# Kernel optimization log

Hardware: AMD Instinct MI355X
Metric: run time of the kernel (lower is better)

Reference implementation:

```python
import jax, jax.numpy as jnp
import numpy as np


def _split_feature(x, ns):
    # channel-last split: [b,h,w,c] -> [b*ns*ns, h/ns, w/ns, c]
    b, h, w, c = x.shape
    hn, wn = h // ns, w // ns
    return x.reshape(b, ns, hn, ns, wn, c).transpose(0, 1, 3, 2, 4, 5).reshape(b * ns * ns, hn, wn, c)


def _merge_splits(x, ns):
    # inverse of _split_feature: [b*ns*ns, h, w, c] -> [b, ns*h, ns*w, c]
    b, h, w, c = x.shape
    nb = b // (ns * ns)
    return x.reshape(nb, ns, ns, h, w, c).transpose(0, 1, 3, 2, 4, 5).reshape(nb, ns * h, ns * w, c)


def _gen_shift_window_attn_mask(h, w, ns):
    # numpy replica of _unimatch_generate_shift_window_attn_mask
    wsh, wsw = h // ns, w // ns
    ssh, ssw = wsh // 2, wsw // 2
    img = np.zeros((1, h, w, 1), dtype=np.float32)
    cnt = 0
    for hs in (slice(0, -wsh), slice(-wsh, -ssh), slice(-ssh, None)):
        for ws in (slice(0, -wsw), slice(-wsw, -ssw), slice(-ssw, None)):
            img[:, hs, ws, :] = cnt
            cnt += 1
    win = img.reshape(1, ns, wsh, ns, wsw, 1).transpose(0, 1, 3, 2, 4, 5).reshape(ns * ns, wsh * wsw)
    am = win[:, None, :] - win[:, :, None]
    return np.where(am != 0, np.float32(-100.0), np.float32(0.0)).astype(np.float32)


def setup_inputs() -> dict:
    key = jax.random.key(0)
    B, H, W, C, NS = 8, 96, 128, 128, 4
    kq, kk, kv = jax.random.split(key, 3)
    q = jax.random.normal(kq, (B, H * W, C), jnp.float32)
    k = jax.random.normal(kk, (B, H * W, C), jnp.float32)
    v = jax.random.normal(kv, (B, H * W, C), jnp.float32)
    attn_mask = jnp.asarray(_gen_shift_window_attn_mask(H, W, NS))  # [NS*NS, n, n]
    return {"q": q, "k": k, "v": v, "attn_mask": attn_mask,
            "num_splits": NS, "with_shift": 1, "h": H, "w": W}


def reference(q, k, v, attn_mask, num_splits, with_shift, h, w):
    b, _, c = q.shape
    ns = num_splits
    wsh, wsw = h // ns, w // ns
    n = wsh * wsw
    bn = b * ns * ns
    q = q.reshape(b, h, w, c)
    k = k.reshape(b, h, w, c)
    v = v.reshape(b, h, w, c)
    if with_shift:
        sh, sw = wsh // 2, wsw // 2
        q = jnp.roll(q, (-sh, -sw), axis=(1, 2))
        k = jnp.roll(k, (-sh, -sw), axis=(1, 2))
        v = jnp.roll(v, (-sh, -sw), axis=(1, 2))
    qf = _split_feature(q, ns).reshape(bn, n, c)
    kf = _split_feature(k, ns).reshape(bn, n, c)
    vf = _split_feature(v, ns).reshape(bn, n, c)
    scale = jnp.asarray(c, qf.dtype) ** 0.5
    scores = jnp.einsum('bnc,bmc->bnm', qf, kf) / scale  # [bn, n, n]
    if with_shift:
        scores = scores + jnp.tile(attn_mask, (b, 1, 1))
    attn = jax.nn.softmax(scores, axis=-1)
    out = jnp.einsum('bnm,bmc->bnc', attn, vf)
    out = _merge_splits(out.reshape(bn, wsh, wsw, c), ns)  # [b, h, w, c]
    if with_shift:
        out = jnp.roll(out, (sh, sw), axis=(1, 2))
    return out.reshape(b, h * w, c)
```

## Files before the change

kernel.cpp:

```cpp
#include <hip/hip_runtime.h>

#define H 96
#define W 128
#define C 128
#define WSH 24
#define WSW 32
#define NTOK 768
#define SH 12
#define SW 16
#define KT 32
#define NKT 24
#define PSTR 40
#define TILE_USH 8192
#define WS_NEED (128L * NKT * TILE_USH * 2)

typedef __attribute__((ext_vector_type(8))) short short8;
typedef __attribute__((ext_vector_type(4))) float floatx4;

__device__ inline unsigned short f2bf(float f) {
  union { float f; unsigned u; } un; un.f = f;
  unsigned r = un.u + 0x7FFF + ((un.u >> 16) & 1);
  return (unsigned short)(r >> 16);
}

__device__ inline int tok_off(int tok, int wh, int ww) {
  int r = tok >> 5;
  int cc = tok & 31;
  int y = wh * WSH + r + SH; if (y >= H) y -= H;
  int x = ww * WSW + cc + SW; if (x >= W) x -= W;
  return y * W + x;
}

__device__ inline void gll16(const void* g, void* lds) {
  __builtin_amdgcn_global_load_lds(
      (const __attribute__((address_space(1))) unsigned int*)g,
      (__attribute__((address_space(3))) unsigned int*)lds, 16, 0, 0);
}

__global__ __launch_bounds__(256) void prep_kernel(const float* __restrict__ k,
                                                   const float* __restrict__ v,
                                                   unsigned short* __restrict__ ws) {
  __shared__ unsigned short Vlds[KT][136];
  const int bid = blockIdx.x;
  const int xcd = bid & 7;
  const int jj = bid >> 3;
  const int w = xcd * 16 + (jj & 15);
  const int kt = jj >> 4;
  const int batch = w >> 4, win = w & 15;
  const int wh = win >> 2, ww = win & 3;
  int y = wh * WSH + kt + SH; if (y >= H) y -= H;

  const int t = threadIdx.x;
  const int key = t >> 3;
  const int j = t & 7;
  const int c0 = j * 16;
  int x = ww * WSW + key + SW; if (x >= W) x -= W;
  const long src = ((long)batch * H * W + (long)y * W + x) * C + c0;
  unsigned short* tile = ws + ((long)w * NKT + kt) * TILE_USH;

  {
    const float* kp = k + src;
    short8 s0, s1;
#pragma unroll
    for (int i = 0; i < 2; ++i) {
      floatx4 a = *(const floatx4*)(kp + i * 8);
      floatx4 b = *(const floatx4*)(kp + i * 8 + 4);
      s0[i*4+0] = (short)f2bf(a[0]); s0[i*4+1] = (short)f2bf(a[1]);
      s0[i*4+2] = (short)f2bf(a[2]); s0[i*4+3] = (short)f2bf(a[3]);
      s1[i*4+0] = (short)f2bf(b[0]); s1[i*4+1] = (short)f2bf(b[1]);
      s1[i*4+2] = (short)f2bf(b[2]); s1[i*4+3] = (short)f2bf(b[3]);
    }
    short8 o0, o1;
    o0[0]=s0[0]; o0[1]=s0[1]; o0[2]=s0[2]; o0[3]=s0[3]; o0[4]=s1[0]; o0[5]=s1[1]; o0[6]=s1[2]; o0[7]=s1[3];
    o1[0]=s0[4]; o1[1]=s0[5]; o1[2]=s0[6]; o1[3]=s0[7]; o1[4]=s1[4]; o1[5]=s1[5]; o1[6]=s1[6]; o1[7]=s1[7];
    const int kc = j >> 1;
    const int q2 = (j & 1) * 2;
    const int half = key >> 4, keyh = key & 15;
    unsigned short* kout = tile + kc * 1024 + half * 512 + keyh * 8;
    *(short8*)(kout + (q2    ) * 128) = o0;
    *(short8*)(kout + (q2 + 1) * 128) = o1;
  }
  {
    const float* vp = v + src;
#pragma unroll
    for (int i = 0; i < 4; ++i) {
      floatx4 a = *(const floatx4*)(vp + i * 4);
      Vlds[key][c0 + i*4 + 0] = f2bf(a[0]);
      Vlds[key][c0 + i*4 + 1] = f2bf(a[1]);
      Vlds[key][c0 + i*4 + 2] = f2bf(a[2]);
      Vlds[key][c0 + i*4 + 3] = f2bf(a[3]);
    }
  }
  __syncthreads();
  {
    const int cb = t >> 5;
    const int rem = t & 31;
    const int col = rem >> 1, qh = rem & 1;
    const int ch = cb * 16 + col;
#pragma unroll
    for (int qs = 0; qs < 2; ++qs) {
      const int quad = qh * 2 + qs;
      short8 o;
#pragma unroll
      for (int i = 0; i < 8; ++i)
        o[i] = (short)Vlds[(i & 1) * 16 + quad * 4 + (i >> 1)][ch];
      *(short8*)(tile + 4096 + cb * 512 + (quad * 16 + col) * 8) = o;
    }
  }
}

__global__ __launch_bounds__(256, 2) void attn_main(const float* __restrict__ q,
                                                    const unsigned short* __restrict__ ws,
                                                    float* __restrict__ out) {
  __shared__ unsigned short Kv[3][TILE_USH];
  __shared__ unsigned short Ps[4][3][16 * PSTR];

  const int bid = blockIdx.x;
  const int x8 = bid & 7;
  const int i = bid >> 3;
  const int w = x8 * 16 + (i & 15);
  const int qb = i >> 4;
  const int batch = w >> 4, win = w & 15;
  const int wh = win >> 2, ww = win & 3;

  const int tid = threadIdx.x;
  const int wv = tid >> 6, lane = tid & 63;
  const int col = lane & 15, quad = lane >> 4;
  const long bbase = (long)batch * (H * W * C);
  const int qbase = qb * 192 + wv * 48;
  const int loff = lane * 8;

  const char* wtile = (const char*)(ws + (long)w * (NKT * TILE_USH));

  auto stage = [&](int buf, int kt) {
    const char* g = wtile + ((long)kt << 14);
#pragma unroll
    for (int c = 0; c < 4; ++c) {
      const int chunk = wv * 4 + c;
      gll16(g + chunk * 1024 + lane * 16, &Kv[buf][chunk * 512]);
    }
  };

  stage(0, 0);
  stage(1, 1);

  short8 qfrag[3][4];
#pragma unroll
  for (int s = 0; s < 3; ++s) {
    const int qtok = qbase + s * 16 + col;
    const float* qp = q + bbase + (long)tok_off(qtok, wh, ww) * C + quad * 8;
#pragma unroll
    for (int kc = 0; kc < 4; ++kc) {
      floatx4 a = *(const floatx4*)(qp + kc * 32);
      floatx4 b = *(const floatx4*)(qp + kc * 32 + 4);
      short8 v8;
      v8[0]=(short)f2bf(a[0]); v8[1]=(short)f2bf(a[1]); v8[2]=(short)f2bf(a[2]); v8[3]=(short)f2bf(a[3]);
      v8[4]=(short)f2bf(b[0]); v8[5]=(short)f2bf(b[1]); v8[6]=(short)f2bf(b[2]); v8[7]=(short)f2bf(b[3]);
      qfrag[s][kc] = v8;
    }
  }

  int qreg[3];
#pragma unroll
  for (int s = 0; s < 3; ++s) {
    int t0 = qbase + s * 16;
    int rr_s = t0 >> 5;
    int qh = (wh == 3) ? ((rr_s >= SH) ? 2 : 1) : 0;
    int qw = (ww == 3) ? ((t0 & 16) ? 2 : 1) : 0;
    qreg[s] = qh * 3 + qw;
  }
  const int cw0 = (ww == 3) ? 1 : 0, cw1 = (ww == 3) ? 2 : 0;
  const float MNEG = -144.2695041f;
  const float SC2 = 0.12751739f;

  floatx4 oacc[3][8];
#pragma unroll
  for (int s = 0; s < 3; ++s)
#pragma unroll
    for (int cb = 0; cb < 8; ++cb) oacc[s][cb] = (floatx4){0.f, 0.f, 0.f, 0.f};
  float lsum[3][4];
#pragma unroll
  for (int s = 0; s < 3; ++s)
#pragma unroll
    for (int r = 0; r < 4; ++r) lsum[s][r] = 0.f;

  asm volatile("s_waitcnt vmcnt(4)" ::: "memory");
  __builtin_amdgcn_s_barrier();

  int cur = 0;
  for (int kt = 0; kt < NKT; ++kt) {
    if (kt + 2 < NKT) {
      int b2 = cur + 2; if (b2 >= 3) b2 -= 3;
      stage(b2, kt + 2);
    }

    short8 kf0[4], kf1[4];
#pragma unroll
    for (int kc = 0; kc < 4; ++kc) {
      kf0[kc] = *(const short8*)&Kv[cur][kc * 1024 + loff];
      kf1[kc] = *(const short8*)&Kv[cur][kc * 1024 + 512 + loff];
    }

    const int khb = (wh == 3) ? ((kt >= SH) ? 6 : 3) : 0;
    const int kr0 = khb + cw0, kr1 = khb + cw1;

    floatx4 A0[3], A1[3];
#pragma unroll
    for (int s = 0; s < 3; ++s) {
      A0[s] = (floatx4){0.f, 0.f, 0.f, 0.f};
      A1[s] = (floatx4){0.f, 0.f, 0.f, 0.f};
    }
    __builtin_amdgcn_s_setprio(1);
#pragma unroll
    for (int kc = 0; kc < 4; ++kc)
#pragma unroll
      for (int s = 0; s < 3; ++s) {
        A0[s] = __builtin_amdgcn_mfma_f32_16x16x32_bf16(qfrag[s][kc], kf0[kc], A0[s], 0, 0, 0);
        A1[s] = __builtin_amdgcn_mfma_f32_16x16x32_bf16(qfrag[s][kc], kf1[kc], A1[s], 0, 0, 0);
      }
    __builtin_amdgcn_s_setprio(0);

    short8 vf[8];
#pragma unroll
    for (int cb = 0; cb < 8; ++cb)
      vf[cb] = *(const short8*)&Kv[cur][4096 + cb * 512 + loff];

    unsigned pkw[3][4];
#pragma unroll
    for (int s = 0; s < 3; ++s) {
      const float m0 = (qreg[s] == kr0) ? 0.f : MNEG;
      const float m1 = (qreg[s] == kr1) ? 0.f : MNEG;
#pragma unroll
      for (int r = 0; r < 4; ++r) {
        float p0 = __builtin_amdgcn_exp2f(fmaf(A0[s][r], SC2, m0));
        float p1 = __builtin_amdgcn_exp2f(fmaf(A1[s][r], SC2, m1));
        lsum[s][r] += p0 + p1;
        pkw[s][r] = (unsigned)f2bf(p0) | ((unsigned)f2bf(p1) << 16);
      }
    }

#pragma unroll
    for (int s = 0; s < 3; ++s)
#pragma unroll
      for (int r = 0; r < 4; ++r)
        *(unsigned*)&Ps[wv][s][(quad * 4 + r) * PSTR + 2 * col] = pkw[s][r];

    short8 pf[3];
#pragma unroll
    for (int s = 0; s < 3; ++s)
      pf[s] = *(const short8*)&Ps[wv][s][col * PSTR + quad * 8];

    __builtin_amdgcn_s_setprio(1);
#pragma unroll
    for (int cb = 0; cb < 8; ++cb)
#pragma unroll
      for (int s = 0; s < 3; ++s)
        oacc[s][cb] = __builtin_amdgcn_mfma_f32_16x16x32_bf16(pf[s], vf[cb], oacc[s][cb], 0, 0, 0);
    __builtin_amdgcn_s_setprio(0);

    if (kt + 1 < NKT) {
      if (kt + 2 < NKT) asm volatile("s_waitcnt vmcnt(4)" ::: "memory");
      else              asm volatile("s_waitcnt vmcnt(0)" ::: "memory");
      __builtin_amdgcn_s_barrier();
    }
    cur += 1; if (cur == 3) cur = 0;
  }

#pragma unroll
  for (int s = 0; s < 3; ++s)
#pragma unroll
    for (int r = 0; r < 4; ++r) {
      float l = lsum[s][r];
      l += __shfl_xor(l, 1); l += __shfl_xor(l, 2);
      l += __shfl_xor(l, 4); l += __shfl_xor(l, 8);
      float inv = 1.0f / l;
      int tok = qbase + s * 16 + quad * 4 + r;
      float* op = out + bbase + (long)tok_off(tok, wh, ww) * C + col;
#pragma unroll
      for (int cb = 0; cb < 8; ++cb) op[cb * 16] = oacc[s][cb][r] * inv;
    }
}

#define KSTRF 136
#define VSTRF 40
#define PSTRF 40
__global__ __launch_bounds__(256, 2) void attn_fallback(
    const float* __restrict__ q, const float* __restrict__ k,
    const float* __restrict__ v, const float* __restrict__ mask,
    float* __restrict__ out) {
  __shared__ unsigned short Ks[KT * KSTRF];
  __shared__ unsigned short Vtl[C * VSTRF];
  __shared__ unsigned short Psf[4][16 * PSTRF];
  const int qtile = blockIdx.x;
  const int beta  = blockIdx.y;
  const int batch = beta >> 4;
  const int win   = beta & 15;
  const int wh = win >> 2, ww = win & 3;
  const int tid = threadIdx.x;
  const int wave = tid >> 6, lane = tid & 63;
  const int col = lane & 15, quad = lane >> 4;
  const long bbase = (long)batch * (H * W * C);
  const int qtok = qtile * 64 + wave * 16 + col;
  const float* qp = q + bbase + (long)tok_off(qtok, wh, ww) * C + quad * 8;
  short8 qfrag[4];
#pragma unroll
  for (int kc = 0; kc < 4; ++kc) {
    floatx4 a = *(const floatx4*)(qp + kc * 32);
    floatx4 b = *(const floatx4*)(qp + kc * 32 + 4);
    short8 s;
    s[0]=f2bf(a[0]); s[1]=f2bf(a[1]); s[2]=f2bf(a[2]); s[3]=f2bf(a[3]);
    s[4]=f2bf(b[0]); s[5]=f2bf(b[1]); s[6]=f2bf(b[2]); s[7]=f2bf(b[3]);
    qfrag[kc] = s;
  }
  floatx4 oacc[8];
#pragma unroll
  for (int i = 0; i < 8; ++i) oacc[i] = (floatx4){0.f,0.f,0.f,0.f};
  float mrow[4], lrow[4];
#pragma unroll
  for (int r = 0; r < 4; ++r) { mrow[r] = -1e30f; lrow[r] = 0.f; }
  const int skey = tid >> 3;
  const int sch  = (tid & 7) * 4;
  const float invscale = 0.088388347648318447f;
  const float* maskw = mask + (long)win * (NTOK * NTOK);
  const int qrow_m = qtile * 64 + wave * 16 + quad * 4;
  for (int kt = 0; kt < NKT; ++kt) {
    const int ktok0 = kt * KT;
    const long srow = bbase + (long)tok_off(ktok0 + skey, wh, ww) * C;
    const float* kp = k + srow;
    const float* vp = v + srow;
    __syncthreads();
#pragma unroll
    for (int j = 0; j < 4; ++j) {
      floatx4 f = *(const floatx4*)(kp + sch + j * 32);
      unsigned lo = (unsigned)f2bf(f[0]) | ((unsigned)f2bf(f[1]) << 16);
      unsigned hi = (unsigned)f2bf(f[2]) | ((unsigned)f2bf(f[3]) << 16);
      *(uint2*)&Ks[skey * KSTRF + sch + j * 32] = make_uint2(lo, hi);
    }
#pragma unroll
    for (int j = 0; j < 4; ++j) {
      floatx4 f = *(const floatx4*)(vp + sch + j * 32);
      int chb = sch + j * 32;
      Vtl[(chb + 0) * VSTRF + skey] = f2bf(f[0]);
      Vtl[(chb + 1) * VSTRF + skey] = f2bf(f[1]);
      Vtl[(chb + 2) * VSTRF + skey] = f2bf(f[2]);
      Vtl[(chb + 3) * VSTRF + skey] = f2bf(f[3]);
    }
    __syncthreads();
    floatx4 s0 = (floatx4){0.f,0.f,0.f,0.f};
    floatx4 s1 = (floatx4){0.f,0.f,0.f,0.f};
#pragma unroll
    for (int kc = 0; kc < 4; ++kc) {
      short8 k0 = *(const short8*)&Ks[col * KSTRF + kc * 32 + quad * 8];
      short8 k1 = *(const short8*)&Ks[(col + 16) * KSTRF + kc * 32 + quad * 8];
      s0 = __builtin_amdgcn_mfma_f32_16x16x32_bf16(qfrag[kc], k0, s0, 0, 0, 0);
      s1 = __builtin_amdgcn_mfma_f32_16x16x32_bf16(qfrag[kc], k1, s1, 0, 0, 0);
    }
    float mk0[4], mk1[4];
    const float* mp = maskw + (long)qrow_m * NTOK + ktok0 + col;
#pragma unroll
    for (int r = 0; r < 4; ++r) { mk0[r] = mp[r * NTOK]; mk1[r] = mp[r * NTOK + 16]; }
#pragma unroll
    for (int r = 0; r < 4; ++r) {
      float a0 = s0[r] * invscale + mk0[r];
      float a1 = s1[r] * invscale + mk1[r];
      float mx = fmaxf(a0, a1);
      mx = fmaxf(mx, __shfl_xor(mx, 1)); mx = fmaxf(mx, __shfl_xor(mx, 2));
      mx = fmaxf(mx, __shfl_xor(mx, 4)); mx = fmaxf(mx, __shfl_xor(mx, 8));
      float mnew = fmaxf(mrow[r], mx);
      float alpha = __expf(mrow[r] - mnew);
      float p0 = __expf(a0 - mnew);
      float p1 = __expf(a1 - mnew);
      float rs = p0 + p1;
      rs += __shfl_xor(rs, 1); rs += __shfl_xor(rs, 2);
      rs += __shfl_xor(rs, 4); rs += __shfl_xor(rs, 8);
      lrow[r] = lrow[r] * alpha + rs;
      mrow[r] = mnew;
#pragma unroll
      for (int cb = 0; cb < 8; ++cb) oacc[cb][r] *= alpha;
      Psf[wave][(quad * 4 + r) * PSTRF + col]      = f2bf(p0);
      Psf[wave][(quad * 4 + r) * PSTRF + 16 + col] = f2bf(p1);
    }
    __syncthreads();
    short8 pf = *(const short8*)&Psf[wave][col * PSTRF + quad * 8];
#pragma unroll
    for (int cb = 0; cb < 8; ++cb) {
      short8 vf = *(const short8*)&Vtl[(cb * 16 + col) * VSTRF + quad * 8];
      oacc[cb] = __builtin_amdgcn_mfma_f32_16x16x32_bf16(pf, vf, oacc[cb], 0, 0, 0);
    }
  }
#pragma unroll
  for (int r = 0; r < 4; ++r) {
    float inv_l = 1.0f / lrow[r];
    int tok = qtile * 64 + wave * 16 + quad * 4 + r;
    float* op = out + bbase + (long)tok_off(tok, wh, ww) * C + col;
#pragma unroll
    for (int cb = 0; cb < 8; ++cb) op[cb * 16] = oacc[cb][r] * inv_l;
  }
}

extern "C" void kernel_launch(void* const* d_in, const int* in_sizes, int n_in,
                              void* d_out, int out_size, void* d_ws, size_t ws_size,
                              hipStream_t stream) {
  const float* q    = (const float*)d_in[0];
  const float* k    = (const float*)d_in[1];
  const float* v    = (const float*)d_in[2];
  const float* mask = (const float*)d_in[3];
  float* out = (float*)d_out;
  if (ws_size >= (size_t)WS_NEED) {
    prep_kernel<<<128 * NKT, 256, 0, stream>>>(k, v, (unsigned short*)d_ws);
    attn_main<<<512, 256, 0, stream>>>(q, (const unsigned short*)d_ws, out);
  } else {
    attn_fallback<<<dim3(12, 128), dim3(256), 0, stream>>>(q, k, v, mask, out);
  }
}
```

Measured before the change: 251.0 us.

## Software-pipeline PV of previous key tile with QK softmax of current tile

Restructures the attention main loop so the P·V MFMAs for tile kt-1 run before the QK and softmax of tile kt. V fragments are held in registers across iterations, and all three K/V buffers are staged up front. The goal is to overlap the exp/softmax VALU work and LDS traffic with matrix-core work, and to remove the dependency stall between QK and PV inside one iteration. The prep kernel also packs V bf16 values into 32-bit LDS stores instead of 16-bit ones. The trade-off is higher register pressure from keeping vf live across iterations, plus extra lgkmcnt waits before each barrier.

```diff
diff --git a/kernel.cpp b/kernel.cpp
--- a/kernel.cpp
+++ b/kernel.cpp
@@ -85,10 +85,10 @@
 #pragma unroll
     for (int i = 0; i < 4; ++i) {
       floatx4 a = *(const floatx4*)(vp + i * 4);
-      Vlds[key][c0 + i*4 + 0] = f2bf(a[0]);
-      Vlds[key][c0 + i*4 + 1] = f2bf(a[1]);
-      Vlds[key][c0 + i*4 + 2] = f2bf(a[2]);
-      Vlds[key][c0 + i*4 + 3] = f2bf(a[3]);
+      unsigned lo = (unsigned)f2bf(a[0]) | ((unsigned)f2bf(a[1]) << 16);
+      unsigned hi = (unsigned)f2bf(a[2]) | ((unsigned)f2bf(a[3]) << 16);
+      *(unsigned*)&Vlds[key][c0 + i*4]     = lo;
+      *(unsigned*)&Vlds[key][c0 + i*4 + 2] = hi;
     }
   }
   __syncthreads();
@@ -141,8 +141,7 @@
     }
   };
 
-  stage(0, 0);
-  stage(1, 1);
+  stage(0, 0); stage(1, 1); stage(2, 2);
 
   short8 qfrag[3][4];
 #pragma unroll
@@ -184,23 +183,13 @@
 #pragma unroll
     for (int r = 0; r < 4; ++r) lsum[s][r] = 0.f;
 
-  asm volatile("s_waitcnt vmcnt(4)" ::: "memory");
-  __builtin_amdgcn_s_barrier();
-
-  int cur = 0;
-  for (int kt = 0; kt < NKT; ++kt) {
-    if (kt + 2 < NKT) {
-      int b2 = cur + 2; if (b2 >= 3) b2 -= 3;
-      stage(b2, kt + 2);
-    }
-
+  auto qk_sm_pw = [&](int kt, int buf) {
     short8 kf0[4], kf1[4];
 #pragma unroll
     for (int kc = 0; kc < 4; ++kc) {
-      kf0[kc] = *(const short8*)&Kv[cur][kc * 1024 + loff];
-      kf1[kc] = *(const short8*)&Kv[cur][kc * 1024 + 512 + loff];
-    }
-
+      kf0[kc] = *(const short8*)&Kv[buf][kc * 1024 + loff];
+      kf1[kc] = *(const short8*)&Kv[buf][kc * 1024 + 512 + loff];
+    }
     const int khb = (wh == 3) ? ((kt >= SH) ? 6 : 3) : 0;
     const int kr0 = khb + cw0, kr1 = khb + cw1;
 
@@ -220,12 +209,6 @@
       }
     __builtin_amdgcn_s_setprio(0);
 
-    short8 vf[8];
-#pragma unroll
-    for (int cb = 0; cb < 8; ++cb)
-      vf[cb] = *(const short8*)&Kv[cur][4096 + cb * 512 + loff];
-
-    unsigned pkw[3][4];
 #pragma unroll
     for (int s = 0; s < 3; ++s) {
       const float m0 = (qreg[s] == kr0) ? 0.f : MNEG;
@@ -235,21 +218,23 @@
         float p0 = __builtin_amdgcn_exp2f(fmaf(A0[s][r], SC2, m0));
         float p1 = __builtin_amdgcn_exp2f(fmaf(A1[s][r], SC2, m1));
         lsum[s][r] += p0 + p1;
-        pkw[s][r] = (unsigned)f2bf(p0) | ((unsigned)f2bf(p1) << 16);
+        unsigned pk = (unsigned)f2bf(p0) | ((unsigned)f2bf(p1) << 16);
+        *(unsigned*)&Ps[wv][s][(quad * 4 + r) * PSTR + 2 * col] = pk;
       }
     }
-
-#pragma unroll
-    for (int s = 0; s < 3; ++s)
-#pragma unroll
-      for (int r = 0; r < 4; ++r)
-        *(unsigned*)&Ps[wv][s][(quad * 4 + r) * PSTR + 2 * col] = pkw[s][r];
-
+  };
+
+  short8 vf[8];
+  auto loadV = [&](int buf) {
+#pragma unroll
+    for (int cb = 0; cb < 8; ++cb)
+      vf[cb] = *(const short8*)&Kv[buf][4096 + cb * 512 + loff];
+  };
+  auto pv = [&]() {
     short8 pf[3];
 #pragma unroll
     for (int s = 0; s < 3; ++s)
       pf[s] = *(const short8*)&Ps[wv][s][col * PSTR + quad * 8];
-
     __builtin_amdgcn_s_setprio(1);
 #pragma unroll
     for (int cb = 0; cb < 8; ++cb)
@@ -257,14 +242,31 @@
       for (int s = 0; s < 3; ++s)
         oacc[s][cb] = __builtin_amdgcn_mfma_f32_16x16x32_bf16(pf[s], vf[cb], oacc[s][cb], 0, 0, 0);
     __builtin_amdgcn_s_setprio(0);
+  };
+
+  asm volatile("s_waitcnt vmcnt(8)" ::: "memory");
+  __builtin_amdgcn_s_barrier();
+
+  qk_sm_pw(0, 0);
+  loadV(0);
+  asm volatile("s_waitcnt vmcnt(4) lgkmcnt(0)" ::: "memory");
+  __builtin_amdgcn_s_barrier();
+
+  for (int kt = 1; kt < NKT; ++kt) {
+    const int buf = kt % 3;
+    if (kt + 2 < NKT) stage((kt + 2) % 3, kt + 2);
+
+    pv();
+    qk_sm_pw(kt, buf);
+    loadV(buf);
 
     if (kt + 1 < NKT) {
-      if (kt + 2 < NKT) asm volatile("s_waitcnt vmcnt(4)" ::: "memory");
-      else              asm volatile("s_waitcnt vmcnt(0)" ::: "memory");
+      if (kt + 2 < NKT) asm volatile("s_waitcnt vmcnt(4) lgkmcnt(0)" ::: "memory");
+      else              asm volatile("s_waitcnt vmcnt(0) lgkmcnt(0)" ::: "memory");
       __builtin_amdgcn_s_barrier();
     }
-    cur += 1; if (cur == 3) cur = 0;
-  }
+  }
+  pv();
 
 #pragma unroll
   for (int s = 0; s < 3; ++s)
```

After: 248.2 us. About the same (-1.1%).
